# Kernel optimization log

Measured on AMD Instinct MI355X. Metric: run time of the kernel, lower is better.

Reference implementation:

```python
import jax, jax.numpy as jnp
import numpy as np

N_ATOMS = 500000
N_BONDS = 1000000
MAX_NB = 6
ATOM_FDIM = 133
BOND_FDIM = 14
HIDDEN = 128
MP_DEPTH = 3
ATOMS_PER_MOL = 20


def setup_inputs() -> dict:
    key = jax.random.key(0)
    ks = jax.random.split(key, 12)
    inp = {
        "f_atoms": jax.random.normal(ks[0], (N_ATOMS, ATOM_FDIM), jnp.float32),
        "f_bonds": jax.random.normal(ks[1], (N_BONDS, BOND_FDIM), jnp.float32),
        "Wi_w": jax.random.normal(ks[2], (HIDDEN, ATOM_FDIM), jnp.float32) * 0.05,
        "Wi_b": jax.random.normal(ks[3], (HIDDEN,), jnp.float32) * 0.05,
        "Wh_w": jax.random.normal(ks[4], (HIDDEN, HIDDEN + BOND_FDIM), jnp.float32) * 0.05,
        "Wh_b": jax.random.normal(ks[5], (HIDDEN,), jnp.float32) * 0.05,
        "Wo_w": jax.random.normal(ks[6], (HIDDEN, ATOM_FDIM + HIDDEN), jnp.float32) * 0.05,
        "Wo_b": jax.random.normal(ks[7], (HIDDEN,), jnp.float32) * 0.05,
        "ffn_w": jax.random.normal(ks[8], (1, HIDDEN), jnp.float32) * 0.05,
        "ffn_b": jax.random.normal(ks[9], (1,), jnp.float32) * 0.05,
        "a2a": jax.random.randint(ks[10], (N_ATOMS, MAX_NB), 0, N_ATOMS, jnp.int32),
        "a2b": jax.random.randint(ks[11], (N_ATOMS, MAX_NB), 0, N_BONDS, jnp.int32),
        "atoms_per_mol": ATOMS_PER_MOL,
    }
    return inp


def reference(f_atoms, f_bonds, Wi_w, Wi_b, Wh_w, Wh_b, Wo_w, Wo_b, ffn_w, ffn_b,
              a2a, a2b, atoms_per_mol):
    # W_i + ReLU: initial atom messages
    x = f_atoms @ Wi_w.T + Wi_b                     # [N_atoms, H]
    message = jax.nn.relu(x)
    # pre-aggregate bond features once (constant across depths)
    nei_f_bonds_sum = f_bonds[a2b].sum(axis=1)      # [N_atoms, BOND_FDIM]
    for _ in range(MP_DEPTH - 1):
        # gather neighbor messages and sum (index_select_ND + sum(dim=1));
        # concat(msg_gather, bond_gather).sum(1) == concat(sum(msg), sum(bond))
        nei_a_message = message[a2a].sum(axis=1)    # [N_atoms, H]
        nei = jnp.concatenate([nei_a_message, nei_f_bonds_sum], axis=1)
        message = jax.nn.relu(x + nei @ Wh_w.T + Wh_b)
        # dropout is identity in eval mode
    # final aggregation + W_o
    a_message = message[a2a].sum(axis=1)            # [N_atoms, H]
    a_input = jnp.concatenate([f_atoms, a_message], axis=1)
    atom_hiddens = jax.nn.relu(a_input @ Wo_w.T + Wo_b)
    # max readout per molecule (equal-size a_scope of atoms_per_mol)
    n_atoms, h = atom_hiddens.shape
    mol_vecs = atom_hiddens.reshape(n_atoms // atoms_per_mol, atoms_per_mol, h).max(axis=1)
    # FFN head (NN_depth=1): Dropout (identity) + Linear(H -> 1)
    return mol_vecs @ ffn_w.T + ffn_b               # [n_mols, 1]
```

## Files before the change

### kernel.cpp

```cpp
#include <hip/hip_runtime.h>
#include <hip/hip_bf16.h>

#define N_ATOMS   500000
#define N_BONDS   1000000
#define MAX_NB    6
#define ATOM_FDIM 133
#define BOND_FDIM 14
#define HIDDEN    128
#define N_MOLS    25000
#define APM       20

typedef __attribute__((ext_vector_type(8))) short short8;
typedef __attribute__((ext_vector_type(4))) float f32x4;
typedef unsigned short u16;
typedef unsigned int   u32;

__device__ __forceinline__ float bf2f(u16 u) {
    u32 t = ((u32)u) << 16;
    return __builtin_bit_cast(float, t);
}
__device__ __forceinline__ u16 f2bf(float f) {
    u32 t = __builtin_bit_cast(u32, f);
    t += 0x7FFFu + ((t >> 16) & 1u);
    return (u16)(t >> 16);
}
__device__ __forceinline__ u32 pk2(float a, float b) {
    return (u32)f2bf(a) | ((u32)f2bf(b) << 16);
}

__device__ __forceinline__ void gl16(const u16* g, u16* l) {
    __builtin_amdgcn_global_load_lds(
        (__attribute__((address_space(1))) void*)(g),
        (__attribute__((address_space(3))) void*)(l), 16, 0, 0);
}

__global__ void prep_weights(const float* __restrict__ Wi, const float* __restrict__ Wh,
                             const float* __restrict__ Wo,
                             u16* __restrict__ Wip, u16* __restrict__ Whp, u16* __restrict__ Wop) {
    int stride = gridDim.x * blockDim.x;
    int tid = blockIdx.x * blockDim.x + threadIdx.x;
    for (int i = tid; i < 128 * 160; i += stride) {
        int r = i / 160, c = i % 160;
        Wip[i] = (c < 133) ? f2bf(Wi[r * 133 + c]) : (u16)0;
        Whp[i] = (c < 142) ? f2bf(Wh[r * 142 + c]) : (u16)0;
    }
    for (int i = tid; i < 128 * 288; i += stride) {
        int r = i / 288, c = i % 288;
        float v = 0.f;
        if (c < 133)      v = Wo[r * 261 + c];
        else if (c >= 160) v = Wo[r * 261 + (c - 27)];
        Wop[i] = f2bf(v);
    }
}

__global__ __launch_bounds__(256) void bond_gather(const float* __restrict__ fb, const int* __restrict__ a2b,
                                                   u16* __restrict__ outp) {
    long t = (long)blockIdx.x * 256 + threadIdx.x;
    int atom = (int)(t >> 4);
    int c2   = (int)(t & 15);
    if (atom >= N_ATOMS) return;
    int c0 = 2 * c2, c1 = c0 + 1;
    float s0 = 0.f, s1 = 0.f;
    if (c0 < BOND_FDIM) {
#pragma unroll
        for (int j = 0; j < MAX_NB; j++) {
            int idx = a2b[atom * 6 + j];
            const float* row = fb + (long)idx * BOND_FDIM;
            s0 += row[c0];
            if (c1 < BOND_FDIM) s1 += row[c1];
        }
    }
    *(u32*)(outp + (long)atom * 32 + c0) = pk2(s0, s1);
}

__global__ __launch_bounds__(256) void gather_relu_sum(const u16* __restrict__ src,
                                                       const int* __restrict__ a2a,
                                                       u16* __restrict__ dst) {
    long t = (long)blockIdx.x * 256 + threadIdx.x;
    int atom = (int)(t >> 4);
    int c8   = (int)(t & 15) << 3;
    float s[8] = {0, 0, 0, 0, 0, 0, 0, 0};
#pragma unroll
    for (int j = 0; j < MAX_NB; j++) {
        int idx = a2a[atom * 6 + j];
        uint4 v = *(const uint4*)(src + (long)idx * 128 + c8);
        u32 w[4] = {v.x, v.y, v.z, v.w};
#pragma unroll
        for (int q = 0; q < 4; q++) {
            s[2 * q]     += fmaxf(__builtin_bit_cast(float, w[q] << 16), 0.f);
            s[2 * q + 1] += fmaxf(__builtin_bit_cast(float, w[q] & 0xFFFF0000u), 0.f);
        }
    }
    uint4 o;
    o.x = pk2(s[0], s[1]);
    o.y = pk2(s[2], s[3]);
    o.z = pk2(s[4], s[5]);
    o.w = pk2(s[6], s[7]);
    *(uint4*)(dst + (long)atom * 128 + c8) = o;
}

#define ISSUE_SLOT(d, t)                                                              \
    do {                                                                              \
        long r_ = (t) * TILE + wave * 16 + lrow;                                      \
        if (r_ > N_ATOMS - 1) r_ = N_ATOMS - 1;                                       \
        if constexpr (KB0 > 0) {                                                      \
            const u16* p_ = A0 + r_ * (long)ldA0 + kg * 8;                            \
            _Pragma("unroll") for (int kb = 0; kb < KB0; kb++)                        \
                a[d][kb] = *(const uint4*)(p_ + kb * 32);                             \
        }                                                                             \
        if constexpr (KB1 > 0) {                                                      \
            const u16* p_ = A1 + r_ * (long)ldA1 + kg * 8;                            \
            _Pragma("unroll") for (int kb = 0; kb < KB1; kb++)                        \
                a[d][KB0 + kb] = *(const uint4*)(p_ + kb * 32);                       \
        }                                                                             \
        if constexpr (ADDX) {                                                         \
            _Pragma("unroll") for (int n = 0; n < 8; n++)                             \
                xv[d][n] = *(const uint2*)(Xadd + r_ * 128 + n * 16 + kg * 4);        \
        }                                                                             \
    } while (0)

template <int KB0, int KB1, bool ADDX, bool BIAS, int DEPTH>
__global__ __launch_bounds__(512, 2) void gemm_rp(
    const u16* __restrict__ A0, int ldA0,
    const u16* __restrict__ A1, int ldA1,
    const u16* __restrict__ Wp, const float* __restrict__ bias,
    const u16* __restrict__ Xadd, u16* __restrict__ Out) {
    constexpr int KB    = KB0 + KB1;
    constexpr int KP    = KB * 32;
    constexpr int TILE  = 128;
    constexpr long NT   = (N_ATOMS + TILE - 1) / TILE;
    constexpr int WSLOTS = KB * 8;
    constexpr int NWAIT = (DEPTH - 1) * (KB + 8 + (ADDX ? 8 : 0));
    static_assert(NWAIT <= 63, "vmcnt range");
    __shared__ __align__(16) u16 WL[WSLOTS * 512];

    const int lane = threadIdx.x & 63;
    const int wave = threadIdx.x >> 6;
    const int lrow = lane & 15;
    const int kg   = lane >> 4;

    for (int s = wave; s < WSLOTS; s += 8) {
        int kb = s >> 3, n = s & 7;
        gl16(Wp + (n * 16 + lrow) * KP + kb * 32 + kg * 8, WL + s * 512);
    }
    asm volatile("s_waitcnt vmcnt(0)" ::: "memory");
    __syncthreads();

    float4 b4[8];
#pragma unroll
    for (int n = 0; n < 8; n++)
        b4[n] = BIAS ? *(const float4*)(bias + n * 16 + kg * 4) : (float4){0.f, 0.f, 0.f, 0.f};

    const int G  = gridDim.x;
    const long t0 = blockIdx.x;

    uint4 a[DEPTH][KB];
    uint2 xv[DEPTH][ADDX ? 8 : 1];

#pragma unroll
    for (int d = 0; d < DEPTH; d++) ISSUE_SLOT(d, t0 + (long)d * G);
    __builtin_amdgcn_sched_barrier(0);

#pragma unroll 1
    for (long tt = t0; tt < NT; tt += (long)DEPTH * G) {
#pragma unroll
        for (int d = 0; d < DEPTH; d++) {
            long t = tt + (long)d * G;
            if (t < NT) {
                asm volatile("s_waitcnt vmcnt(%0)" :: "n"(NWAIT) : "memory");
                __builtin_amdgcn_sched_barrier(0);

                f32x4 acc[8];
#pragma unroll
                for (int n = 0; n < 8; n++) acc[n] = (f32x4){0.f, 0.f, 0.f, 0.f};
#pragma unroll
                for (int kb = 0; kb < KB; kb++) {
                    short8 af = __builtin_bit_cast(short8, a[d][kb]);
#pragma unroll
                    for (int n = 0; n < 8; n++) {
                        short8 bf = *(const short8*)(WL + (kb * 8 + n) * 512 + lane * 8);
                        acc[n] = __builtin_amdgcn_mfma_f32_16x16x32_bf16(bf, af, acc[n], 0, 0, 0);
                    }
                }

                long r = t * TILE + wave * 16 + lrow;
                if (r < N_ATOMS) {
#pragma unroll
                    for (int n = 0; n < 8; n++) {
                        float v0 = acc[n][0] + b4[n].x;
                        float v1 = acc[n][1] + b4[n].y;
                        float v2 = acc[n][2] + b4[n].z;
                        float v3 = acc[n][3] + b4[n].w;
                        if constexpr (ADDX) {
                            v0 += __builtin_bit_cast(float, xv[d][n].x << 16);
                            v1 += __builtin_bit_cast(float, xv[d][n].x & 0xFFFF0000u);
                            v2 += __builtin_bit_cast(float, xv[d][n].y << 16);
                            v3 += __builtin_bit_cast(float, xv[d][n].y & 0xFFFF0000u);
                        }
                        uint2 o;
                        o.x = pk2(v0, v1);
                        o.y = pk2(v2, v3);
                        *(uint2*)(Out + r * 128 + n * 16 + kg * 4) = o;
                    }
                }
                __builtin_amdgcn_sched_barrier(0);
                ISSUE_SLOT(d, t + (long)DEPTH * G);
                __builtin_amdgcn_sched_barrier(0);
            }
        }
    }
}

__global__ __launch_bounds__(512, 2) void gemm_wi(
    const float* __restrict__ FA, const u16* __restrict__ Wp,
    const float* __restrict__ bias, u16* __restrict__ fa16, u16* __restrict__ Out) {
    constexpr int KB = 5, KP = 160, TILE = 128;
    constexpr long NT = (N_ATOMS + TILE - 1) / TILE;
    constexpr int WSLOTS = KB * 8;
    constexpr int DEPTH = 2;
    constexpr int NWAIT = 23;
    __shared__ __align__(16) u16 WL[WSLOTS * 512];

    const int lane = threadIdx.x & 63;
    const int wave = threadIdx.x >> 6;
    const int lrow = lane & 15;
    const int kg   = lane >> 4;

    for (int s = wave; s < WSLOTS; s += 8) {
        int kb = s >> 3, n = s & 7;
        gl16(Wp + (n * 16 + lrow) * KP + kb * 32 + kg * 8, WL + s * 512);
    }
    asm volatile("s_waitcnt vmcnt(0)" ::: "memory");
    __syncthreads();

    float4 b4[8];
#pragma unroll
    for (int n = 0; n < 8; n++) b4[n] = *(const float4*)(bias + n * 16 + kg * 4);

    const int G  = gridDim.x;
    const long t0 = blockIdx.x;

    uint4 af32[DEPTH][4][2];
    uint4 a4[DEPTH];
    float a4s[DEPTH];

#define WI_ISSUE(d, t)                                                         \
    do {                                                                       \
        long r_ = (t) * TILE + wave * 16 + lrow;                               \
        if (r_ > N_ATOMS - 1) r_ = N_ATOMS - 1;                                \
        const float* p_ = FA + r_ * (long)ATOM_FDIM + kg * 8;                  \
        _Pragma("unroll") for (int kb = 0; kb < 4; kb++) {                     \
            af32[d][kb][0] = *(const uint4*)(p_ + kb * 32);                    \
            af32[d][kb][1] = *(const uint4*)(p_ + kb * 32 + 4);                \
        }                                                                      \
        if (kg == 0) {                                                         \
            const float* q_ = FA + r_ * (long)ATOM_FDIM + 128;                 \
            a4[d]  = *(const uint4*)(q_);                                      \
            a4s[d] = q_[4];                                                    \
        }                                                                      \
    } while (0)

#pragma unroll
    for (int d = 0; d < DEPTH; d++) WI_ISSUE(d, t0 + (long)d * G);
    __builtin_amdgcn_sched_barrier(0);

#pragma unroll 1
    for (long tt = t0; tt < NT; tt += (long)DEPTH * G) {
#pragma unroll
        for (int d = 0; d < DEPTH; d++) {
            long t = tt + (long)d * G;
            if (t < NT) {
                asm volatile("s_waitcnt vmcnt(%0)" :: "n"(NWAIT) : "memory");
                __builtin_amdgcn_sched_barrier(0);

                long r = t * TILE + wave * 16 + lrow;
                bool wr = (r < N_ATOMS);

                short8 frag[5];
#pragma unroll
                for (int kb = 0; kb < 4; kb++) {
                    float f[8];
                    f[0] = __builtin_bit_cast(float4, af32[d][kb][0]).x;
                    f[1] = __builtin_bit_cast(float4, af32[d][kb][0]).y;
                    f[2] = __builtin_bit_cast(float4, af32[d][kb][0]).z;
                    f[3] = __builtin_bit_cast(float4, af32[d][kb][0]).w;
                    f[4] = __builtin_bit_cast(float4, af32[d][kb][1]).x;
                    f[5] = __builtin_bit_cast(float4, af32[d][kb][1]).y;
                    f[6] = __builtin_bit_cast(float4, af32[d][kb][1]).z;
                    f[7] = __builtin_bit_cast(float4, af32[d][kb][1]).w;
                    uint4 pk;
                    pk.x = pk2(f[0], f[1]);
                    pk.y = pk2(f[2], f[3]);
                    pk.z = pk2(f[4], f[5]);
                    pk.w = pk2(f[6], f[7]);
                    frag[kb] = __builtin_bit_cast(short8, pk);
                }
                {
                    uint4 pk = (uint4){0, 0, 0, 0};
                    if (kg == 0) {
                        float4 q = __builtin_bit_cast(float4, a4[d]);
                        pk.x = pk2(q.x, q.y);
                        pk.y = pk2(q.z, q.w);
                        pk.z = pk2(a4s[d], 0.f);
                        pk.w = 0;
                    }
                    frag[4] = __builtin_bit_cast(short8, pk);
                }

                f32x4 acc[8];
#pragma unroll
                for (int n = 0; n < 8; n++) acc[n] = (f32x4){0.f, 0.f, 0.f, 0.f};
#pragma unroll
                for (int kb = 0; kb < 5; kb++) {
#pragma unroll
                    for (int n = 0; n < 8; n++) {
                        short8 bf = *(const short8*)(WL + (kb * 8 + n) * 512 + lane * 8);
                        acc[n] = __builtin_amdgcn_mfma_f32_16x16x32_bf16(bf, frag[kb], acc[n], 0, 0, 0);
                    }
                }

                if (wr) {
#pragma unroll
                    for (int kb = 0; kb < 5; kb++)
                        *(uint4*)(fa16 + r * 160 + kb * 32 + kg * 8) = __builtin_bit_cast(uint4, frag[kb]);
#pragma unroll
                    for (int n = 0; n < 8; n++) {
                        uint2 o;
                        o.x = pk2(acc[n][0] + b4[n].x, acc[n][1] + b4[n].y);
                        o.y = pk2(acc[n][2] + b4[n].z, acc[n][3] + b4[n].w);
                        *(uint2*)(Out + r * 128 + n * 16 + kg * 4) = o;
                    }
                }
                __builtin_amdgcn_sched_barrier(0);
                WI_ISSUE(d, t + (long)DEPTH * G);
                __builtin_amdgcn_sched_barrier(0);
            }
        }
    }
#undef WI_ISSUE
}

__global__ __launch_bounds__(256) void readout(const u16* __restrict__ ah,
                                               const float* __restrict__ ffn_w,
                                               const float* __restrict__ ffn_b,
                                               float* __restrict__ out) {
    int mol  = blockIdx.x * 4 + (threadIdx.x >> 6);
    int lane = threadIdx.x & 63;
    if (mol >= N_MOLS) return;
    float m0 = -1e30f, m1 = -1e30f;
    const u16* base = ah + (long)mol * APM * 128 + 2 * lane;
#pragma unroll
    for (int a = 0; a < APM; a++) {
        u32 v = *(const u32*)(base + a * 128);
        m0 = fmaxf(m0, bf2f((u16)(v & 0xFFFFu)));
        m1 = fmaxf(m1, bf2f((u16)(v >> 16)));
    }
    m0 = fmaxf(m0, 0.f);
    m1 = fmaxf(m1, 0.f);
    float p = m0 * ffn_w[2 * lane] + m1 * ffn_w[2 * lane + 1];
#pragma unroll
    for (int off = 32; off > 0; off >>= 1) p += __shfl_down(p, off);
    if (lane == 0) out[mol] = p + ffn_b[0];
}

extern "C" void kernel_launch(void* const* d_in, const int* in_sizes, int n_in,
                              void* d_out, int out_size, void* d_ws, size_t ws_size,
                              hipStream_t stream) {
    const float* f_atoms = (const float*)d_in[0];
    const float* f_bonds = (const float*)d_in[1];
    const float* Wi_w = (const float*)d_in[2];
    const float* Wi_b = (const float*)d_in[3];
    const float* Wh_w = (const float*)d_in[4];
    const float* Wh_b = (const float*)d_in[5];
    const float* Wo_w = (const float*)d_in[6];
    const float* Wo_b = (const float*)d_in[7];
    const float* ffn_w = (const float*)d_in[8];
    const float* ffn_b = (const float*)d_in[9];
    const int* a2a = (const int*)d_in[10];
    const int* a2b = (const int*)d_in[11];
    float* out = (float*)d_out;

    char* ws = (char*)d_ws;
    u16* fa    = (u16*)(ws);
    u16* xb    = (u16*)(ws + 160000000L);
    u16* msgA  = (u16*)(ws + 288000000L);
    u16* msgB  = (u16*)(ws + 416000000L);
    u16* nsum  = (u16*)(ws + 544000000L);
    u16* nbond = (u16*)(ws + 672000000L);
    u16* Wip   = (u16*)(ws + 704000000L);
    u16* Whp   = (u16*)(ws + 704040960L);
    u16* Wop   = (u16*)(ws + 704081920L);

    prep_weights<<<64, 256, 0, stream>>>(Wi_w, Wh_w, Wo_w, Wip, Whp, Wop);
    bond_gather<<<31250, 256, 0, stream>>>(f_bonds, a2b, nbond);

    gemm_wi<<<256, 512, 0, stream>>>(f_atoms, Wip, Wi_b, fa, xb);

    gather_relu_sum<<<31250, 256, 0, stream>>>(xb, a2a, nsum);
    gemm_rp<4, 1, true, true, 4><<<256, 512, 0, stream>>>(
        nsum, 128, nbond, 32, Whp, Wh_b, xb, msgA);
    gather_relu_sum<<<31250, 256, 0, stream>>>(msgA, a2a, nsum);
    gemm_rp<4, 1, true, true, 4><<<256, 512, 0, stream>>>(
        nsum, 128, nbond, 32, Whp, Wh_b, xb, msgB);
    gather_relu_sum<<<31250, 256, 0, stream>>>(msgB, a2a, nsum);
    gemm_rp<5, 4, false, true, 3><<<256, 512, 0, stream>>>(
        fa, 160, nsum, 128, Wop, Wo_b, (const u16*)nullptr, msgA);

    readout<<<6250, 256, 0, stream>>>(msgA, ffn_w, ffn_b, out);
}
```

Before: 873.8 us.

## Replace software-pipelined GEMM loops with simple per-wave tiles and more occupancy

Drops the manual multi-stage register prefetch and vmcnt pipelining in the dense GEMM kernels. Each wave now loads its 16-row tile, computes and stores it, and latency is hidden by running more waves (256-thread blocks, 4 blocks per CU, 1024 blocks). This trades explicit prefetch and register use for thread-level parallelism. It also rereads the bias per tile instead of keeping it in registers, and each block redoes its weight staging into LDS, so there are more such preloads with more blocks.

```diff
diff --git a/kernel.cpp b/kernel.cpp
--- a/kernel.cpp
+++ b/kernel.cpp
@@ -99,39 +99,16 @@
     *(uint4*)(dst + (long)atom * 128 + c8) = o;
 }
 
-#define ISSUE_SLOT(d, t)                                                              \
-    do {                                                                              \
-        long r_ = (t) * TILE + wave * 16 + lrow;                                      \
-        if (r_ > N_ATOMS - 1) r_ = N_ATOMS - 1;                                       \
-        if constexpr (KB0 > 0) {                                                      \
-            const u16* p_ = A0 + r_ * (long)ldA0 + kg * 8;                            \
-            _Pragma("unroll") for (int kb = 0; kb < KB0; kb++)                        \
-                a[d][kb] = *(const uint4*)(p_ + kb * 32);                             \
-        }                                                                             \
-        if constexpr (KB1 > 0) {                                                      \
-            const u16* p_ = A1 + r_ * (long)ldA1 + kg * 8;                            \
-            _Pragma("unroll") for (int kb = 0; kb < KB1; kb++)                        \
-                a[d][KB0 + kb] = *(const uint4*)(p_ + kb * 32);                       \
-        }                                                                             \
-        if constexpr (ADDX) {                                                         \
-            _Pragma("unroll") for (int n = 0; n < 8; n++)                             \
-                xv[d][n] = *(const uint2*)(Xadd + r_ * 128 + n * 16 + kg * 4);        \
-        }                                                                             \
-    } while (0)
-
-template <int KB0, int KB1, bool ADDX, bool BIAS, int DEPTH>
-__global__ __launch_bounds__(512, 2) void gemm_rp(
+template <int KB0, int KB1, bool ADDX, bool BIAS>
+__global__ __launch_bounds__(256, 4) void gemm_tlp(
     const u16* __restrict__ A0, int ldA0,
     const u16* __restrict__ A1, int ldA1,
     const u16* __restrict__ Wp, const float* __restrict__ bias,
     const u16* __restrict__ Xadd, u16* __restrict__ Out) {
-    constexpr int KB    = KB0 + KB1;
-    constexpr int KP    = KB * 32;
-    constexpr int TILE  = 128;
-    constexpr long NT   = (N_ATOMS + TILE - 1) / TILE;
+    constexpr int KB = KB0 + KB1;
+    constexpr int KP = KB * 32;
     constexpr int WSLOTS = KB * 8;
-    constexpr int NWAIT = (DEPTH - 1) * (KB + 8 + (ADDX ? 8 : 0));
-    static_assert(NWAIT <= 63, "vmcnt range");
+    constexpr long NTILE = N_ATOMS / 16;
     __shared__ __align__(16) u16 WL[WSLOTS * 512];
 
     const int lane = threadIdx.x & 63;
@@ -139,86 +116,76 @@
     const int lrow = lane & 15;
     const int kg   = lane >> 4;
 
-    for (int s = wave; s < WSLOTS; s += 8) {
+    for (int s = wave; s < WSLOTS; s += 4) {
         int kb = s >> 3, n = s & 7;
         gl16(Wp + (n * 16 + lrow) * KP + kb * 32 + kg * 8, WL + s * 512);
     }
     asm volatile("s_waitcnt vmcnt(0)" ::: "memory");
     __syncthreads();
 
-    float4 b4[8];
-#pragma unroll
-    for (int n = 0; n < 8; n++)
-        b4[n] = BIAS ? *(const float4*)(bias + n * 16 + kg * 4) : (float4){0.f, 0.f, 0.f, 0.f};
-
-    const int G  = gridDim.x;
-    const long t0 = blockIdx.x;
-
-    uint4 a[DEPTH][KB];
-    uint2 xv[DEPTH][ADDX ? 8 : 1];
-
-#pragma unroll
-    for (int d = 0; d < DEPTH; d++) ISSUE_SLOT(d, t0 + (long)d * G);
-    __builtin_amdgcn_sched_barrier(0);
-
+    const long TW = (long)gridDim.x * 4;
 #pragma unroll 1
-    for (long tt = t0; tt < NT; tt += (long)DEPTH * G) {
-#pragma unroll
-        for (int d = 0; d < DEPTH; d++) {
-            long t = tt + (long)d * G;
-            if (t < NT) {
-                asm volatile("s_waitcnt vmcnt(%0)" :: "n"(NWAIT) : "memory");
-                __builtin_amdgcn_sched_barrier(0);
-
-                f32x4 acc[8];
-#pragma unroll
-                for (int n = 0; n < 8; n++) acc[n] = (f32x4){0.f, 0.f, 0.f, 0.f};
-#pragma unroll
-                for (int kb = 0; kb < KB; kb++) {
-                    short8 af = __builtin_bit_cast(short8, a[d][kb]);
-#pragma unroll
-                    for (int n = 0; n < 8; n++) {
-                        short8 bf = *(const short8*)(WL + (kb * 8 + n) * 512 + lane * 8);
-                        acc[n] = __builtin_amdgcn_mfma_f32_16x16x32_bf16(bf, af, acc[n], 0, 0, 0);
-                    }
-                }
-
-                long r = t * TILE + wave * 16 + lrow;
-                if (r < N_ATOMS) {
-#pragma unroll
-                    for (int n = 0; n < 8; n++) {
-                        float v0 = acc[n][0] + b4[n].x;
-                        float v1 = acc[n][1] + b4[n].y;
-                        float v2 = acc[n][2] + b4[n].z;
-                        float v3 = acc[n][3] + b4[n].w;
-                        if constexpr (ADDX) {
-                            v0 += __builtin_bit_cast(float, xv[d][n].x << 16);
-                            v1 += __builtin_bit_cast(float, xv[d][n].x & 0xFFFF0000u);
-                            v2 += __builtin_bit_cast(float, xv[d][n].y << 16);
-                            v3 += __builtin_bit_cast(float, xv[d][n].y & 0xFFFF0000u);
-                        }
-                        uint2 o;
-                        o.x = pk2(v0, v1);
-                        o.y = pk2(v2, v3);
-                        *(uint2*)(Out + r * 128 + n * 16 + kg * 4) = o;
-                    }
-                }
-                __builtin_amdgcn_sched_barrier(0);
-                ISSUE_SLOT(d, t + (long)DEPTH * G);
-                __builtin_amdgcn_sched_barrier(0);
-            }
-        }
-    }
-}
-
-__global__ __launch_bounds__(512, 2) void gemm_wi(
+    for (long tile = (long)blockIdx.x * 4 + wave; tile < NTILE; tile += TW) {
+        const long r = tile * 16 + lrow;
+
+        uint4 a[KB];
+        if constexpr (KB0 > 0) {
+            const u16* p = A0 + r * (long)ldA0 + kg * 8;
+#pragma unroll
+            for (int kb = 0; kb < KB0; kb++) a[kb] = *(const uint4*)(p + kb * 32);
+        }
+        if constexpr (KB1 > 0) {
+            const u16* p = A1 + r * (long)ldA1 + kg * 8;
+#pragma unroll
+            for (int kb = 0; kb < KB1; kb++) a[KB0 + kb] = *(const uint4*)(p + kb * 32);
+        }
+        uint2 xv[ADDX ? 8 : 1];
+        if constexpr (ADDX) {
+#pragma unroll
+            for (int n = 0; n < 8; n++)
+                xv[n] = *(const uint2*)(Xadd + r * 128 + n * 16 + kg * 4);
+        }
+
+        f32x4 acc[8];
+#pragma unroll
+        for (int n = 0; n < 8; n++) acc[n] = (f32x4){0.f, 0.f, 0.f, 0.f};
+#pragma unroll
+        for (int kb = 0; kb < KB; kb++) {
+            short8 af = __builtin_bit_cast(short8, a[kb]);
+#pragma unroll
+            for (int n = 0; n < 8; n++) {
+                short8 bf = *(const short8*)(WL + (kb * 8 + n) * 512 + lane * 8);
+                acc[n] = __builtin_amdgcn_mfma_f32_16x16x32_bf16(bf, af, acc[n], 0, 0, 0);
+            }
+        }
+
+#pragma unroll
+        for (int n = 0; n < 8; n++) {
+            float v0 = acc[n][0], v1 = acc[n][1], v2 = acc[n][2], v3 = acc[n][3];
+            if constexpr (BIAS) {
+                float4 b4 = *(const float4*)(bias + n * 16 + kg * 4);
+                v0 += b4.x; v1 += b4.y; v2 += b4.z; v3 += b4.w;
+            }
+            if constexpr (ADDX) {
+                v0 += __builtin_bit_cast(float, xv[n].x << 16);
+                v1 += __builtin_bit_cast(float, xv[n].x & 0xFFFF0000u);
+                v2 += __builtin_bit_cast(float, xv[n].y << 16);
+                v3 += __builtin_bit_cast(float, xv[n].y & 0xFFFF0000u);
+            }
+            uint2 o;
+            o.x = pk2(v0, v1);
+            o.y = pk2(v2, v3);
+            *(uint2*)(Out + r * 128 + n * 16 + kg * 4) = o;
+        }
+    }
+}
+
+__global__ __launch_bounds__(256, 4) void gemm_wi(
     const float* __restrict__ FA, const u16* __restrict__ Wp,
     const float* __restrict__ bias, u16* __restrict__ fa16, u16* __restrict__ Out) {
-    constexpr int KB = 5, KP = 160, TILE = 128;
-    constexpr long NT = (N_ATOMS + TILE - 1) / TILE;
+    constexpr int KB = 5, KP = 160;
     constexpr int WSLOTS = KB * 8;
-    constexpr int DEPTH = 2;
-    constexpr int NWAIT = 23;
+    constexpr long NTILE = N_ATOMS / 16;
     __shared__ __align__(16) u16 WL[WSLOTS * 512];
 
     const int lane = threadIdx.x & 63;
@@ -226,118 +193,80 @@
     const int lrow = lane & 15;
     const int kg   = lane >> 4;
 
-    for (int s = wave; s < WSLOTS; s += 8) {
+    for (int s = wave; s < WSLOTS; s += 4) {
         int kb = s >> 3, n = s & 7;
         gl16(Wp + (n * 16 + lrow) * KP + kb * 32 + kg * 8, WL + s * 512);
     }
     asm volatile("s_waitcnt vmcnt(0)" ::: "memory");
     __syncthreads();
 
-    float4 b4[8];
-#pragma unroll
-    for (int n = 0; n < 8; n++) b4[n] = *(const float4*)(bias + n * 16 + kg * 4);
-
-    const int G  = gridDim.x;
-    const long t0 = blockIdx.x;
-
-    uint4 af32[DEPTH][4][2];
-    uint4 a4[DEPTH];
-    float a4s[DEPTH];
-
-#define WI_ISSUE(d, t)                                                         \
-    do {                                                                       \
-        long r_ = (t) * TILE + wave * 16 + lrow;                               \
-        if (r_ > N_ATOMS - 1) r_ = N_ATOMS - 1;                                \
-        const float* p_ = FA + r_ * (long)ATOM_FDIM + kg * 8;                  \
-        _Pragma("unroll") for (int kb = 0; kb < 4; kb++) {                     \
-            af32[d][kb][0] = *(const uint4*)(p_ + kb * 32);                    \
-            af32[d][kb][1] = *(const uint4*)(p_ + kb * 32 + 4);                \
-        }                                                                      \
-        if (kg == 0) {                                                         \
-            const float* q_ = FA + r_ * (long)ATOM_FDIM + 128;                 \
-            a4[d]  = *(const uint4*)(q_);                                      \
-            a4s[d] = q_[4];                                                    \
-        }                                                                      \
-    } while (0)
-
-#pragma unroll
-    for (int d = 0; d < DEPTH; d++) WI_ISSUE(d, t0 + (long)d * G);
-    __builtin_amdgcn_sched_barrier(0);
-
+    const long TW = (long)gridDim.x * 4;
 #pragma unroll 1
-    for (long tt = t0; tt < NT; tt += (long)DEPTH * G) {
-#pragma unroll
-        for (int d = 0; d < DEPTH; d++) {
-            long t = tt + (long)d * G;
-            if (t < NT) {
-                asm volatile("s_waitcnt vmcnt(%0)" :: "n"(NWAIT) : "memory");
-                __builtin_amdgcn_sched_barrier(0);
-
-                long r = t * TILE + wave * 16 + lrow;
-                bool wr = (r < N_ATOMS);
-
-                short8 frag[5];
-#pragma unroll
-                for (int kb = 0; kb < 4; kb++) {
-                    float f[8];
-                    f[0] = __builtin_bit_cast(float4, af32[d][kb][0]).x;
-                    f[1] = __builtin_bit_cast(float4, af32[d][kb][0]).y;
-                    f[2] = __builtin_bit_cast(float4, af32[d][kb][0]).z;
-                    f[3] = __builtin_bit_cast(float4, af32[d][kb][0]).w;
-                    f[4] = __builtin_bit_cast(float4, af32[d][kb][1]).x;
-                    f[5] = __builtin_bit_cast(float4, af32[d][kb][1]).y;
-                    f[6] = __builtin_bit_cast(float4, af32[d][kb][1]).z;
-                    f[7] = __builtin_bit_cast(float4, af32[d][kb][1]).w;
-                    uint4 pk;
-                    pk.x = pk2(f[0], f[1]);
-                    pk.y = pk2(f[2], f[3]);
-                    pk.z = pk2(f[4], f[5]);
-                    pk.w = pk2(f[6], f[7]);
-                    frag[kb] = __builtin_bit_cast(short8, pk);
-                }
-                {
-                    uint4 pk = (uint4){0, 0, 0, 0};
-                    if (kg == 0) {
-                        float4 q = __builtin_bit_cast(float4, a4[d]);
-                        pk.x = pk2(q.x, q.y);
-                        pk.y = pk2(q.z, q.w);
-                        pk.z = pk2(a4s[d], 0.f);
-                        pk.w = 0;
-                    }
-                    frag[4] = __builtin_bit_cast(short8, pk);
-                }
-
-                f32x4 acc[8];
-#pragma unroll
-                for (int n = 0; n < 8; n++) acc[n] = (f32x4){0.f, 0.f, 0.f, 0.f};
-#pragma unroll
-                for (int kb = 0; kb < 5; kb++) {
-#pragma unroll
-                    for (int n = 0; n < 8; n++) {
-                        short8 bf = *(const short8*)(WL + (kb * 8 + n) * 512 + lane * 8);
-                        acc[n] = __builtin_amdgcn_mfma_f32_16x16x32_bf16(bf, frag[kb], acc[n], 0, 0, 0);
-                    }
-                }
-
-                if (wr) {
-#pragma unroll
-                    for (int kb = 0; kb < 5; kb++)
-                        *(uint4*)(fa16 + r * 160 + kb * 32 + kg * 8) = __builtin_bit_cast(uint4, frag[kb]);
-#pragma unroll
-                    for (int n = 0; n < 8; n++) {
-                        uint2 o;
-                        o.x = pk2(acc[n][0] + b4[n].x, acc[n][1] + b4[n].y);
-                        o.y = pk2(acc[n][2] + b4[n].z, acc[n][3] + b4[n].w);
-                        *(uint2*)(Out + r * 128 + n * 16 + kg * 4) = o;
-                    }
-                }
-                __builtin_amdgcn_sched_barrier(0);
-                WI_ISSUE(d, t + (long)DEPTH * G);
-                __builtin_amdgcn_sched_barrier(0);
-            }
-        }
-    }
-#undef WI_ISSUE
+    for (long tile = (long)blockIdx.x * 4 + wave; tile < NTILE; tile += TW) {
+        const long r = tile * 16 + lrow;
+        const float* p = FA + r * (long)ATOM_FDIM + kg * 8;
+
+        uint4 af32[4][2];
+#pragma unroll
+        for (int kb = 0; kb < 4; kb++) {
+            af32[kb][0] = *(const uint4*)(p + kb * 32);
+            af32[kb][1] = *(const uint4*)(p + kb * 32 + 4);
+        }
+        uint4 a4 = (uint4){0, 0, 0, 0};
+        float a4s = 0.f;
+        if (kg == 0) {
+            const float* q = FA + r * (long)ATOM_FDIM + 128;
+            a4  = *(const uint4*)(q);
+            a4s = q[4];
+        }
+
+        short8 frag[5];
+#pragma unroll
+        for (int kb = 0; kb < 4; kb++) {
+            float4 lo = __builtin_bit_cast(float4, af32[kb][0]);
+            float4 hi = __builtin_bit_cast(float4, af32[kb][1]);
+            uint4 pk;
+            pk.x = pk2(lo.x, lo.y);
+            pk.y = pk2(lo.z, lo.w);
+            pk.z = pk2(hi.x, hi.y);
+            pk.w = pk2(hi.z, hi.w);
+            frag[kb] = __builtin_bit_cast(short8, pk);
+        }
+        {
+            uint4 pk = (uint4){0, 0, 0, 0};
+            if (kg == 0) {
+                float4 q = __builtin_bit_cast(float4, a4);
+                pk.x = pk2(q.x, q.y);
+                pk.y = pk2(q.z, q.w);
+                pk.z = pk2(a4s, 0.f);
+            }
+            frag[4] = __builtin_bit_cast(short8, pk);
+        }
+
+        f32x4 acc[8];
+#pragma unroll
+        for (int n = 0; n < 8; n++) acc[n] = (f32x4){0.f, 0.f, 0.f, 0.f};
+#pragma unroll
+        for (int kb = 0; kb < 5; kb++) {
+#pragma unroll
+            for (int n = 0; n < 8; n++) {
+                short8 bf = *(const short8*)(WL + (kb * 8 + n) * 512 + lane * 8);
+                acc[n] = __builtin_amdgcn_mfma_f32_16x16x32_bf16(bf, frag[kb], acc[n], 0, 0, 0);
+            }
+        }
+
+#pragma unroll
+        for (int kb = 0; kb < 5; kb++)
+            *(uint4*)(fa16 + r * 160 + kb * 32 + kg * 8) = __builtin_bit_cast(uint4, frag[kb]);
+#pragma unroll
+        for (int n = 0; n < 8; n++) {
+            float4 b4 = *(const float4*)(bias + n * 16 + kg * 4);
+            uint2 o;
+            o.x = pk2(acc[n][0] + b4.x, acc[n][1] + b4.y);
+            o.y = pk2(acc[n][2] + b4.z, acc[n][3] + b4.w);
+            *(uint2*)(Out + r * 128 + n * 16 + kg * 4) = o;
+        }
+    }
 }
 
 __global__ __launch_bounds__(256) void readout(const u16* __restrict__ ah,
@@ -394,16 +323,16 @@
     prep_weights<<<64, 256, 0, stream>>>(Wi_w, Wh_w, Wo_w, Wip, Whp, Wop);
     bond_gather<<<31250, 256, 0, stream>>>(f_bonds, a2b, nbond);
 
-    gemm_wi<<<256, 512, 0, stream>>>(f_atoms, Wip, Wi_b, fa, xb);
+    gemm_wi<<<1024, 256, 0, stream>>>(f_atoms, Wip, Wi_b, fa, xb);
 
     gather_relu_sum<<<31250, 256, 0, stream>>>(xb, a2a, nsum);
-    gemm_rp<4, 1, true, true, 4><<<256, 512, 0, stream>>>(
+    gemm_tlp<4, 1, true, true><<<1024, 256, 0, stream>>>(
         nsum, 128, nbond, 32, Whp, Wh_b, xb, msgA);
     gather_relu_sum<<<31250, 256, 0, stream>>>(msgA, a2a, nsum);
-    gemm_rp<4, 1, true, true, 4><<<256, 512, 0, stream>>>(
+    gemm_tlp<4, 1, true, true><<<1024, 256, 0, stream>>>(
         nsum, 128, nbond, 32, Whp, Wh_b, xb, msgB);
     gather_relu_sum<<<31250, 256, 0, stream>>>(msgB, a2a, nsum);
-    gemm_rp<5, 4, false, true, 3><<<256, 512, 0, stream>>>(
+    gemm_tlp<5, 4, false, true><<<1024, 256, 0, stream>>>(
         fa, 160, nsum, 128, Wop, Wo_b, (const u16*)nullptr, msgA);
 
     readout<<<6250, 256, 0, stream>>>(msgA, ffn_w, ffn_b, out);
```

After: 1.494 ms. +70.9%, slower.
